# Performance work log

Hardware: AMD Instinct MI355X
Metric: run time of the kernel (lower is better)

Reference implementation:

```python
import jax, jax.numpy as jnp
import numpy as np

B, L, F = 16, 1080, 2
D = 128          # d_model
NC = 64          # num_cnn_channels
DIN = 256        # expand * d_model
N = 16           # d_state
K = 4            # d_conv
R = 8            # dt_rank = ceil(d_model/16)
OUT = 3
NB = 3           # num_mamba_blocks


def setup_inputs() -> dict:
    key = jax.random.key(0)
    ks = jax.random.split(key, 24)
    nrm = lambda k, shape, s=0.05: (jax.random.normal(k, shape) * s).astype(jnp.float32)
    bn = lambda c: jnp.stack([jnp.ones(c), jnp.zeros(c), jnp.zeros(c), jnp.ones(c)]).astype(jnp.float32)
    return {
        'x': jax.random.normal(ks[0], (B, L, F), dtype=jnp.float32),
        'emb_W': nrm(ks[1], (F, D), 0.5), 'emb_b': jnp.zeros(D, jnp.float32),
        'c3_W': nrm(ks[2], (NC, D, 3)), 'c3_b': jnp.zeros(NC, jnp.float32), 'bn3': bn(NC),
        'c5_W': nrm(ks[3], (NC, D, 5)), 'c5_b': jnp.zeros(NC, jnp.float32), 'bn5': bn(NC),
        'c7_W': nrm(ks[4], (NC, D, 7)), 'c7_b': jnp.zeros(NC, jnp.float32), 'bn7': bn(NC),
        'cf_W': nrm(ks[5], (D, 3 * NC, 1)), 'cf_b': jnp.zeros(D, jnp.float32), 'bnf': bn(D),
        'ln_g': jnp.ones((NB, D), jnp.float32), 'ln_b': jnp.zeros((NB, D), jnp.float32),
        'in_W': nrm(ks[6], (NB, 2 * DIN, D)),
        'mconv_W': nrm(ks[7], (NB, DIN, K), 0.2), 'mconv_b': jnp.zeros((NB, DIN), jnp.float32),
        'xproj_W': nrm(ks[8], (NB, R + 2 * N, DIN)),
        'dt_W': nrm(ks[9], (NB, DIN, R), 0.1), 'dt_b': jnp.full((NB, DIN), -1.0, jnp.float32),
        'A_log': jnp.tile(jnp.log(jnp.arange(1.0, N + 1.0, dtype=jnp.float32)), (NB, DIN, 1)),
        'Dp': jnp.ones((NB, DIN), jnp.float32),
        'out_W': nrm(ks[10], (NB, D, DIN)),
        'flin_W': nrm(ks[11], (D, 2 * D)), 'flin_b': jnp.zeros(D, jnp.float32),
        'fc_W': nrm(ks[12], (OUT, D)), 'fc_b': jnp.zeros(OUT, jnp.float32),
    }


def conv1d(x, W, b, pad):
    # x: (B,C,L), W: (O,C,K)
    y = jax.lax.conv_general_dilated(x, W, (1,), [(pad, pad)],
                                     dimension_numbers=('NCH', 'OIH', 'NCH'))
    return y + b[None, :, None]


def bn_relu(x, bn, eps=1e-5):
    g, b, m, v = bn  # each (C,)
    return jax.nn.relu((x - m[None, :, None]) * (g / jnp.sqrt(v + eps))[None, :, None] + b[None, :, None])


def layernorm(x, g, b, eps=1e-5):
    mu = x.mean(-1, keepdims=True)
    var = ((x - mu) ** 2).mean(-1, keepdims=True)
    return (x - mu) / jnp.sqrt(var + eps) * g + b


def pos_encoding(seq_len, d_model):
    pos = jnp.arange(seq_len, dtype=jnp.float32)[:, None]
    div = jnp.exp(jnp.arange(0, d_model, 2, dtype=jnp.float32) * (-np.log(10000.0) / d_model))
    pe = jnp.zeros((seq_len, d_model), jnp.float32)
    pe = pe.at[:, 0::2].set(jnp.sin(pos * div)).at[:, 1::2].set(jnp.cos(pos * div))
    return pe


def selective_scan(u, dt, A, Bm, Cm, Dp):
    # u,dt: (b,l,d); A: (d,n); Bm,Cm: (b,l,n); Dp: (d,)
    dA = jnp.exp(dt[..., None] * A)                    # (b,l,d,n)
    dBu = (dt * u)[..., None] * Bm[:, :, None, :]      # (b,l,d,n)

    def step(h, t):
        dA_t, dBu_t, C_t = t
        h = dA_t * h + dBu_t                           # (b,d,n)
        return h, jnp.einsum('bdn,bn->bd', h, C_t)

    h0 = jnp.zeros((u.shape[0], u.shape[2], A.shape[1]), u.dtype)
    _, ys = jax.lax.scan(step, h0, (jnp.swapaxes(dA, 0, 1), jnp.swapaxes(dBu, 0, 1), jnp.swapaxes(Cm, 0, 1)))
    return jnp.swapaxes(ys, 0, 1) + u * Dp


def mamba_block(x, in_W, conv_W, conv_b, xproj_W, dt_W, dt_b, A_log, Dp, out_W):
    xz = x @ in_W.T                                    # (b,l,2*din)
    xs, z = jnp.split(xz, 2, axis=-1)
    xc = jnp.swapaxes(xs, 1, 2)                        # (b,din,l)
    xc = jax.lax.conv_general_dilated(xc, conv_W[:, None, :], (1,), [(K - 1, 0)],
                                      dimension_numbers=('NCH', 'OIH', 'NCH'),
                                      feature_group_count=DIN)
    u = jax.nn.silu(jnp.swapaxes(xc + conv_b[None, :, None], 1, 2))  # (b,l,din)
    dbl = u @ xproj_W.T
    dt, Bm, Cm = dbl[..., :R], dbl[..., R:R + N], dbl[..., R + N:]
    dt = jax.nn.softplus(dt @ dt_W.T + dt_b)
    A = -jnp.exp(A_log)
    y = selective_scan(u, dt, A, Bm, Cm, Dp)
    return (y * jax.nn.silu(z)) @ out_W.T


def reference(x, emb_W, emb_b, c3_W, c3_b, bn3, c5_W, c5_b, bn5, c7_W, c7_b, bn7,
              cf_W, cf_b, bnf, ln_g, ln_b, in_W, mconv_W, mconv_b, xproj_W,
              dt_W, dt_b, A_log, Dp, out_W, flin_W, flin_b, fc_W, fc_b):
    xe = x @ emb_W + emb_b + pos_encoding(x.shape[1], emb_W.shape[1])  # (B,L,D)
    ci = jnp.swapaxes(xe, 1, 2)                                        # (B,D,L)
    o3 = bn_relu(conv1d(ci, c3_W, c3_b, 1), bn3)
    o5 = bn_relu(conv1d(ci, c5_W, c5_b, 2), bn5)
    o7 = bn_relu(conv1d(ci, c7_W, c7_b, 3), bn7)
    cc = jnp.concatenate([o3, o5, o7], axis=1)                         # (B,3*NC,L)
    cf = bn_relu(conv1d(cc, cf_W, cf_b, 0), bnf)
    cnn_feat = jnp.swapaxes(cf, 1, 2)                                  # (B,L,D)
    m = xe
    for i in range(NB):  # Sequential(LN, Mamba, Dropout) -- no residual, dropout=eval
        m = mamba_block(layernorm(m, ln_g[i], ln_b[i]), in_W[i], mconv_W[i], mconv_b[i],
                        xproj_W[i], dt_W[i], dt_b[i], A_log[i], Dp[i], out_W[i])
    fused = jax.nn.relu(jnp.concatenate([cnn_feat, m], axis=-1) @ flin_W.T + flin_b)
    pooled = fused.mean(axis=1)                                        # AdaptiveAvgPool1d(1)
    return pooled @ fc_W.T + fc_b
```

## Files before the change

kernel.cpp:

```cpp
#include <hip/hip_runtime.h>
#include <math.h>

#define LSEQ   1080
#define NBATCH 16
#define BLROWS (LSEQ*NBATCH)
#define CHN    27
#define LCH    40

typedef __bf16  bf16x8 __attribute__((ext_vector_type(8)));
typedef float   f32x4  __attribute__((ext_vector_type(4)));
typedef short   short8 __attribute__((ext_vector_type(8)));
typedef short   short4v __attribute__((ext_vector_type(4)));

__device__ __forceinline__ float silu_f(float x) { return x / (1.f + __expf(-x)); }

__device__ __forceinline__ unsigned short f2bf(float f) {
    unsigned int u = __float_as_uint(f);
    u += 0x7fffu + ((u >> 16) & 1u);
    return (unsigned short)(u >> 16);
}
__device__ __forceinline__ float bf2f(unsigned short h) {
    return __uint_as_float(((unsigned int)h) << 16);
}

__global__ __launch_bounds__(256) void embed_kernel(
    const float* __restrict__ x, const float* __restrict__ embW,
    const float* __restrict__ embb, float* __restrict__ xe)
{
    int idx = blockIdx.x * 256 + threadIdx.x;
    if (idx >= BLROWS * 128) return;
    int d = idx & 127;
    int r = idx >> 7;
    int t = r % LSEQ;
    float x0 = x[(size_t)r * 2], x1 = x[(size_t)r * 2 + 1];
    int i2 = d & 126;
    float div = expf((float)i2 * (-9.210340371976184f / 128.f));
    float arg = (float)t * div;
    float pe = (d & 1) ? cosf(arg) : sinf(arg);
    xe[idx] = fmaf(x0, embW[d], fmaf(x1, embW[128 + d], embb[d] + pe));
}

__global__ __launch_bounds__(256) void convw_kernel(
    const float* __restrict__ src, unsigned short* __restrict__ dh,
    unsigned short* __restrict__ dl, int NBk, int N, int Npad, int K)
{
    int idx = blockIdx.x * 256 + threadIdx.x;
    int total = NBk * Npad * K;
    if (idx >= total) return;
    int k = idx % K;
    int n = (idx / K) % Npad;
    int blk = idx / (K * Npad);
    float v = (n < N) ? src[((size_t)blk * N + n) * K + k] : 0.f;
    unsigned short h = f2bf(v);
    dh[idx] = h;
    dl[idx] = f2bf(v - bf2f(h));
}

__global__ __launch_bounds__(256) void convw_conv_kernel(
    const float* __restrict__ src, unsigned short* __restrict__ dh,
    unsigned short* __restrict__ dl, int T)
{
    int idx = blockIdx.x * 256 + threadIdx.x;
    int total = 64 * 128 * T;
    if (idx >= total) return;
    int kk = idx % (128 * T);
    int n = idx / (128 * T);
    int tap = kk / 128, d = kk % 128;
    float v = src[((size_t)n * 128 + d) * T + tap];
    unsigned short h = f2bf(v);
    dh[idx] = h;
    dl[idx] = f2bf(v - bf2f(h));
}

template<int BM, int BN>
__global__ __launch_bounds__(256) void gemm_mfma(
    const float* __restrict__ A, int lda,
    const unsigned short* __restrict__ Wh, const unsigned short* __restrict__ Wl,
    int Ntot, int Kd, int KT, int pad,
    const float* __restrict__ bias, const float* __restrict__ bn, int bnN, int epi,
    float* __restrict__ C, int ldc)
{
    constexpr int WM = BM / 2, WN = BN / 2;
    constexpr int MR = WM / 16, NR = WN / 16;
    constexpr int LA = (BM * 8) / 256;
    constexpr int LB = (BN * 4) / 256;

    __shared__ unsigned short Ah[BM][40], Al[BM][40];
    __shared__ unsigned short Bh[BN][40], Bl[BN][40];

    const int tid = threadIdx.x;
    const int b  = blockIdx.z;
    const int t0 = blockIdx.y * BM;
    const int n0 = blockIdx.x * BN;
    const float* Ab = A + (size_t)b * LSEQ * lda;
    const int wrow = Kd * KT;

    const int lane = tid & 63, wid = tid >> 6;
    const int wr = wid >> 1, wc = wid & 1;
    const int fr = lane & 15, fq = lane >> 4;

    f32x4 acc[MR][NR];
#pragma unroll
    for (int m = 0; m < MR; ++m)
#pragma unroll
        for (int n = 0; n < NR; ++n) acc[m][n] = (f32x4){0.f, 0.f, 0.f, 0.f};

    for (int tap = 0; tap < KT; ++tap) {
        const int shift = tap - pad;
        for (int ks = 0; ks < Kd; ks += 32) {
#pragma unroll
            for (int l = 0; l < LA; ++l) {
                int c = tid + l * 256;
                int row = c >> 3, kc = (c & 7) << 2;
                int ts = t0 + row + shift;
                float4 av = make_float4(0.f, 0.f, 0.f, 0.f);
                if (ts >= 0 && ts < LSEQ)
                    av = *(const float4*)(Ab + (size_t)ts * lda + ks + kc);
                alignas(8) unsigned short hs[4], ls[4];
                float fv[4] = {av.x, av.y, av.z, av.w};
#pragma unroll
                for (int j = 0; j < 4; ++j) {
                    unsigned short h = f2bf(fv[j]);
                    hs[j] = h;
                    ls[j] = f2bf(fv[j] - bf2f(h));
                }
                *(short4v*)&Ah[row][kc] = *(short4v*)hs;
                *(short4v*)&Al[row][kc] = *(short4v*)ls;
            }
            const int kglob = tap * Kd + ks;
#pragma unroll
            for (int l = 0; l < LB; ++l) {
                int c = tid + l * 256;
                int col = c >> 2, kc = (c & 3) << 3;
                size_t src = (size_t)(n0 + col) * wrow + kglob + kc;
                *(short8*)&Bh[col][kc] = *(const short8*)&Wh[src];
                *(short8*)&Bl[col][kc] = *(const short8*)&Wl[src];
            }
            __syncthreads();
            bf16x8 bhf[NR], blf[NR];
#pragma unroll
            for (int n = 0; n < NR; ++n) {
                int colr = wc * WN + n * 16 + fr;
                bhf[n] = __builtin_bit_cast(bf16x8, *(const short8*)&Bh[colr][fq * 8]);
                blf[n] = __builtin_bit_cast(bf16x8, *(const short8*)&Bl[colr][fq * 8]);
            }
#pragma unroll
            for (int m = 0; m < MR; ++m) {
                int rowr = wr * WM + m * 16 + fr;
                bf16x8 ahf = __builtin_bit_cast(bf16x8, *(const short8*)&Ah[rowr][fq * 8]);
                bf16x8 alf = __builtin_bit_cast(bf16x8, *(const short8*)&Al[rowr][fq * 8]);
#pragma unroll
                for (int n = 0; n < NR; ++n) {
                    acc[m][n] = __builtin_amdgcn_mfma_f32_16x16x32_bf16(ahf, bhf[n], acc[m][n], 0, 0, 0);
                    acc[m][n] = __builtin_amdgcn_mfma_f32_16x16x32_bf16(ahf, blf[n], acc[m][n], 0, 0, 0);
                    acc[m][n] = __builtin_amdgcn_mfma_f32_16x16x32_bf16(alf, bhf[n], acc[m][n], 0, 0, 0);
                }
            }
            __syncthreads();
        }
    }

    float* Cb = C + (size_t)b * LSEQ * ldc;
#pragma unroll
    for (int m = 0; m < MR; ++m) {
#pragma unroll
        for (int n = 0; n < NR; ++n) {
            int colg = n0 + wc * WN + n * 16 + fr;
            if (colg >= Ntot) continue;
#pragma unroll
            for (int r = 0; r < 4; ++r) {
                int t = t0 + wr * WM + m * 16 + fq * 4 + r;
                if (t >= LSEQ) continue;
                float v = acc[m][n][r];
                if (epi == 1) {
                    v += bias[colg];
                    float gg = bn[colg], bb = bn[bnN + colg];
                    float mm = bn[2 * bnN + colg], vv = bn[3 * bnN + colg];
                    v = (v - mm) * (gg / sqrtf(vv + 1e-5f)) + bb;
                    v = v > 0.f ? v : 0.f;
                } else if (epi == 2) {
                    v += bias[colg];
                    v = v > 0.f ? v : 0.f;
                }
                Cb[(size_t)t * ldc + colg] = v;
            }
        }
    }
}

__global__ __launch_bounds__(256) void ln_kernel(
    const float* __restrict__ in, const float* __restrict__ g,
    const float* __restrict__ b2, float* __restrict__ out)
{
    int lane = threadIdx.x & 63;
    int wid  = threadIdx.x >> 6;
    int row = blockIdx.x * 4 + wid;
    if (row >= BLROWS) return;
    const float* rp = in + (size_t)row * 128;
    float v0 = rp[lane], v1 = rp[lane + 64];
    float s = v0 + v1;
#pragma unroll
    for (int o2 = 32; o2 > 0; o2 >>= 1) s += __shfl_xor(s, o2, 64);
    float mu = s * (1.f / 128.f);
    float d0 = v0 - mu, d1 = v1 - mu;
    float q = d0 * d0 + d1 * d1;
#pragma unroll
    for (int o2 = 32; o2 > 0; o2 >>= 1) q += __shfl_xor(q, o2, 64);
    float rs = 1.f / sqrtf(q * (1.f / 128.f) + 1e-5f);
    float* op = out + (size_t)row * 128;
    op[lane]      = d0 * rs * g[lane]      + b2[lane];
    op[lane + 64] = d1 * rs * g[lane + 64] + b2[lane + 64];
}

__global__ __launch_bounds__(256) void mconv_kernel(
    const float* __restrict__ xz, const float* __restrict__ Wc,
    const float* __restrict__ bc, float* __restrict__ u)
{
    int idx = blockIdx.x * 256 + threadIdx.x;
    int c = idx & 255;
    int r = idx >> 8;
    if (r >= BLROWS) return;
    int t = r % LSEQ;
    const float* xs = xz + (size_t)r * 512 + c;
    float acc = bc[c];
    if (t >= 3) acc = fmaf(xs[-3 * 512], Wc[c * 4 + 0], acc);
    if (t >= 2) acc = fmaf(xs[-2 * 512], Wc[c * 4 + 1], acc);
    if (t >= 1) acc = fmaf(xs[-1 * 512], Wc[c * 4 + 2], acc);
    acc = fmaf(xs[0], Wc[c * 4 + 3], acc);
    u[(size_t)r * 256 + c] = silu_f(acc);
}

__global__ __launch_bounds__(256) void dtk_kernel(
    const float* __restrict__ dbl, const float* __restrict__ dtW,
    const float* __restrict__ dtb, float* __restrict__ dtout)
{
    int idx = blockIdx.x * 256 + threadIdx.x;
    int c = idx & 255;
    int r = idx >> 8;
    if (r >= BLROWS) return;
    const float* dr = dbl + (size_t)r * 40;
    float a = dtb[c];
#pragma unroll
    for (int j = 0; j < 8; ++j) a = fmaf(dr[j], dtW[c * 8 + j], a);
    float sp = (a > 20.f) ? a : log1pf(__expf(a));
    dtout[(size_t)r * 256 + c] = sp;
}

__global__ __launch_bounds__(256) void scan1_kernel(
    const float* __restrict__ dt, const float* __restrict__ u,
    const float* __restrict__ dbl, const float* __restrict__ Alog,
    float* __restrict__ P, float* __restrict__ S)
{
    int idx = blockIdx.x * 256 + threadIdx.x;
    int d = idx & 255;
    int rest = idx >> 8;
    int ch = rest % CHN;
    int b  = rest / CHN;
    float A2[16];
#pragma unroll
    for (int n = 0; n < 16; ++n) A2[n] = -__expf(Alog[d * 16 + n]);
    float p[16], s[16];
#pragma unroll
    for (int n = 0; n < 16; ++n) { p[n] = 1.f; s[n] = 0.f; }
    int r0 = b * LSEQ + ch * LCH;
    for (int q = 0; q < LCH; ++q) {
        size_t r = (size_t)(r0 + q);
        float dtv = dt[r * 256 + d];
        float uv  = u [r * 256 + d];
        float dtu = dtv * uv;
        const float* Br = dbl + r * 40 + 8;
#pragma unroll
        for (int n = 0; n < 16; ++n) {
            float a = __expf(dtv * A2[n]);
            p[n] *= a;
            s[n] = fmaf(a, s[n], dtu * Br[n]);
        }
    }
    size_t ob = ((size_t)(b * CHN + ch) * 256 + d) * 16;
#pragma unroll
    for (int n = 0; n < 16; ++n) { P[ob + n] = p[n]; S[ob + n] = s[n]; }
}

__global__ __launch_bounds__(256) void scan2_kernel(
    const float* __restrict__ P, const float* __restrict__ S, float* __restrict__ H0)
{
    int idx = blockIdx.x * 256 + threadIdx.x;
    int n = idx & 15;
    int d = (idx >> 4) & 255;
    int b = idx >> 12;
    float h = 0.f;
    for (int ch = 0; ch < CHN; ++ch) {
        size_t o = ((size_t)(b * CHN + ch) * 256 + d) * 16 + n;
        H0[o] = h;
        h = fmaf(P[o], h, S[o]);
    }
}

__global__ __launch_bounds__(256) void scan3_kernel(
    const float* __restrict__ dt, const float* __restrict__ u,
    const float* __restrict__ dbl, const float* __restrict__ Alog,
    const float* __restrict__ H0, const float* __restrict__ Dp,
    const float* __restrict__ xz, float* __restrict__ g)
{
    int idx = blockIdx.x * 256 + threadIdx.x;
    int d = idx & 255;
    int rest = idx >> 8;
    int ch = rest % CHN;
    int b  = rest / CHN;
    float A2[16];
#pragma unroll
    for (int n = 0; n < 16; ++n) A2[n] = -__expf(Alog[d * 16 + n]);
    float h[16];
    size_t ob = ((size_t)(b * CHN + ch) * 256 + d) * 16;
#pragma unroll
    for (int n = 0; n < 16; ++n) h[n] = H0[ob + n];
    float Dpd = Dp[d];
    int r0 = b * LSEQ + ch * LCH;
    for (int q = 0; q < LCH; ++q) {
        size_t r = (size_t)(r0 + q);
        float dtv = dt[r * 256 + d];
        float uv  = u [r * 256 + d];
        float dtu = dtv * uv;
        const float* Br = dbl + r * 40 + 8;
        const float* Cr = dbl + r * 40 + 24;
        float acc = 0.f;
#pragma unroll
        for (int n = 0; n < 16; ++n) {
            float a = __expf(dtv * A2[n]);
            h[n] = fmaf(a, h[n], dtu * Br[n]);
            acc = fmaf(h[n], Cr[n], acc);
        }
        float yv = fmaf(uv, Dpd, acc);
        float zv = xz[r * 512 + 256 + d];
        g[r * 256 + d] = yv * silu_f(zv);
    }
}

__global__ __launch_bounds__(128) void pool1_kernel(
    const float* __restrict__ fused, float* __restrict__ part)
{
    int d = threadIdx.x;
    int blk = blockIdx.x;
    int ch = blk % CHN;
    int b  = blk / CHN;
    int t0 = ch * LCH;
    float s = 0.f;
    for (int q = 0; q < LCH; ++q)
        s += fused[((size_t)(b * LSEQ + t0 + q)) * 128 + d];
    part[(size_t)(b * CHN + ch) * 128 + d] = s;
}

__global__ __launch_bounds__(128) void pool2_kernel(
    const float* __restrict__ part, const float* __restrict__ fcW,
    const float* __restrict__ fcb, float* __restrict__ out)
{
    __shared__ float pl[128];
    int d = threadIdx.x;
    int b = blockIdx.x;
    float s = 0.f;
    for (int ch = 0; ch < CHN; ++ch) s += part[(size_t)(b * CHN + ch) * 128 + d];
    pl[d] = s * (1.f / 1080.f);
    __syncthreads();
    if (d < 3) {
        float a = fcb[d];
        for (int dd = 0; dd < 128; ++dd) a = fmaf(pl[dd], fcW[d * 128 + dd], a);
        out[b * 3 + d] = a;
    }
}

extern "C" void kernel_launch(void* const* d_in, const int* in_sizes, int n_in,
                              void* d_out, int out_size, void* d_ws, size_t ws_size,
                              hipStream_t stream)
{
    const float* x    = (const float*)d_in[0];
    const float* embW = (const float*)d_in[1];
    const float* embb = (const float*)d_in[2];
    const float* c3W  = (const float*)d_in[3];
    const float* c3b  = (const float*)d_in[4];
    const float* bn3  = (const float*)d_in[5];
    const float* c5W  = (const float*)d_in[6];
    const float* c5b  = (const float*)d_in[7];
    const float* bn5  = (const float*)d_in[8];
    const float* c7W  = (const float*)d_in[9];
    const float* c7b  = (const float*)d_in[10];
    const float* bn7  = (const float*)d_in[11];
    const float* cfW  = (const float*)d_in[12];
    const float* cfb  = (const float*)d_in[13];
    const float* bnf  = (const float*)d_in[14];
    const float* lng  = (const float*)d_in[15];
    const float* lnb  = (const float*)d_in[16];
    const float* inW  = (const float*)d_in[17];
    const float* mcW  = (const float*)d_in[18];
    const float* mcb  = (const float*)d_in[19];
    const float* xpW  = (const float*)d_in[20];
    const float* dtW  = (const float*)d_in[21];
    const float* dtbp = (const float*)d_in[22];
    const float* Alog = (const float*)d_in[23];
    const float* Dp   = (const float*)d_in[24];
    const float* outW = (const float*)d_in[25];
    const float* flW  = (const float*)d_in[26];
    const float* flb  = (const float*)d_in[27];
    const float* fcW  = (const float*)d_in[28];
    const float* fcb  = (const float*)d_in[29];

    float* ws = (float*)d_ws;
    size_t off = 0;
    auto alloc = [&](size_t n) { float* p = ws + off; off += n; return p; };
    float* xe   = alloc((size_t)BLROWS * 128);
    float* lnx  = alloc((size_t)BLROWS * 128);
    float* xz   = alloc((size_t)BLROWS * 512);
    float* ub   = alloc((size_t)BLROWS * 256);
    float* dtt  = alloc((size_t)BLROWS * 256);
    float* dbl  = alloc((size_t)BLROWS * 40);
    float* gb   = alloc((size_t)BLROWS * 256);
    float* mbuf = alloc((size_t)BLROWS * 128);
    float* fin  = alloc((size_t)BLROWS * 256);
    float* Pb   = alloc((size_t)NBATCH * CHN * 256 * 16);
    float* Sb   = alloc((size_t)NBATCH * CHN * 256 * 16);
    float* h0b  = alloc((size_t)NBATCH * CHN * 256 * 16);
    float* cc    = gb;
    float* fused = lnx;

    off = (off + 3) & ~(size_t)3;
    unsigned short* us = (unsigned short*)(ws + off);
    size_t uo = 0;
    auto ualloc = [&](size_t n) { unsigned short* p = us + uo; uo += n; return p; };
    unsigned short* c3h = ualloc(64 * 384);  unsigned short* c3l = ualloc(64 * 384);
    unsigned short* c5h = ualloc(64 * 640);  unsigned short* c5l = ualloc(64 * 640);
    unsigned short* c7h = ualloc(64 * 896);  unsigned short* c7l = ualloc(64 * 896);
    unsigned short* cfh = ualloc(128 * 192); unsigned short* cfl = ualloc(128 * 192);
    unsigned short* inh = ualloc((size_t)1536 * 128); unsigned short* inl = ualloc((size_t)1536 * 128);
    unsigned short* xph = ualloc((size_t)3 * 64 * 256); unsigned short* xpl = ualloc((size_t)3 * 64 * 256);
    unsigned short* oth = ualloc((size_t)384 * 256); unsigned short* otl = ualloc((size_t)384 * 256);
    unsigned short* flh = ualloc((size_t)128 * 256); unsigned short* fll = ualloc((size_t)128 * 256);
    (void)ws_size; (void)in_sizes; (void)n_in; (void)out_size;

    convw_conv_kernel<<<(64 * 384 + 255) / 256, 256, 0, stream>>>(c3W, c3h, c3l, 3);
    convw_conv_kernel<<<(64 * 640 + 255) / 256, 256, 0, stream>>>(c5W, c5h, c5l, 5);
    convw_conv_kernel<<<(64 * 896 + 255) / 256, 256, 0, stream>>>(c7W, c7h, c7l, 7);
    convw_kernel<<<(128 * 192 + 255) / 256, 256, 0, stream>>>(cfW, cfh, cfl, 1, 128, 128, 192);
    convw_kernel<<<(1536 * 128 + 255) / 256, 256, 0, stream>>>(inW, inh, inl, 1, 1536, 1536, 128);
    convw_kernel<<<(3 * 64 * 256 + 255) / 256, 256, 0, stream>>>(xpW, xph, xpl, 3, 40, 64, 256);
    convw_kernel<<<(384 * 256 + 255) / 256, 256, 0, stream>>>(outW, oth, otl, 1, 384, 384, 256);
    convw_kernel<<<(128 * 256 + 255) / 256, 256, 0, stream>>>(flW, flh, fll, 1, 128, 128, 256);

    embed_kernel<<<(BLROWS * 128) / 256, 256, 0, stream>>>(x, embW, embb, xe);

    dim3 g64(1, 17, NBATCH);
    gemm_mfma<64, 64><<<g64, 256, 0, stream>>>(xe, 128, c3h, c3l, 64, 128, 3, 1,
                                               c3b, bn3, 64, 1, cc, 192);
    gemm_mfma<64, 64><<<g64, 256, 0, stream>>>(xe, 128, c5h, c5l, 64, 128, 5, 2,
                                               c5b, bn5, 64, 1, cc + 64, 192);
    gemm_mfma<64, 64><<<g64, 256, 0, stream>>>(xe, 128, c7h, c7l, 64, 128, 7, 3,
                                               c7b, bn7, 64, 1, cc + 128, 192);
    dim3 g128(1, 17, NBATCH);
    gemm_mfma<64, 128><<<g128, 256, 0, stream>>>(cc, 192, cfh, cfl, 128, 192, 1, 0,
                                                 cfb, bnf, 128, 1, fin, 256);

    for (int i = 0; i < 3; ++i) {
        const float* min_ = (i == 0) ? xe : ((i == 1) ? mbuf : xe);
        float* mout = (i == 0) ? mbuf : ((i == 1) ? xe : (fin + 128));
        int ldout = (i < 2) ? 128 : 256;

        ln_kernel<<<BLROWS / 4, 256, 0, stream>>>(min_, lng + i * 128, lnb + i * 128, lnx);

        dim3 gin(4, 17, NBATCH);
        gemm_mfma<64, 128><<<gin, 256, 0, stream>>>(lnx, 128, inh + (size_t)i * 512 * 128,
                                                    inl + (size_t)i * 512 * 128,
                                                    512, 128, 1, 0, nullptr, nullptr, 0, 0,
                                                    xz, 512);

        mconv_kernel<<<BLROWS, 256, 0, stream>>>(xz, mcW + i * 256 * 4, mcb + i * 256, ub);

        gemm_mfma<64, 64><<<g64, 256, 0, stream>>>(ub, 256, xph + (size_t)i * 64 * 256,
                                                   xpl + (size_t)i * 64 * 256,
                                                   40, 256, 1, 0, nullptr, nullptr, 0, 0,
                                                   dbl, 40);

        dtk_kernel<<<BLROWS, 256, 0, stream>>>(dbl, dtW + i * 256 * 8, dtbp + i * 256, dtt);

        scan1_kernel<<<(NBATCH * 256 * CHN) / 256, 256, 0, stream>>>(
            dtt, ub, dbl, Alog + i * 256 * 16, Pb, Sb);
        scan2_kernel<<<(NBATCH * 256 * 16) / 256, 256, 0, stream>>>(Pb, Sb, h0b);
        scan3_kernel<<<(NBATCH * 256 * CHN) / 256, 256, 0, stream>>>(
            dtt, ub, dbl, Alog + i * 256 * 16, h0b, Dp + i * 256, xz, gb);

        gemm_mfma<64, 128><<<g128, 256, 0, stream>>>(gb, 256, oth + (size_t)i * 128 * 256,
                                                     otl + (size_t)i * 128 * 256,
                                                     128, 256, 1, 0, nullptr, nullptr, 0, 0,
                                                     mout, ldout);
    }

    gemm_mfma<64, 128><<<g128, 256, 0, stream>>>(fin, 256, flh, fll, 128, 256, 1, 0,
                                                 flb, nullptr, 0, 2, fused, 128);

    pool1_kernel<<<NBATCH * CHN, 128, 0, stream>>>(fused, Pb);
    pool2_kernel<<<NBATCH, 128, 0, stream>>>(Pb, fcW, fcb, (float*)d_out);
}
```

Measured before the change: 795.8 us.

## Split scan state across 4 lanes, merge weight-convert and conv launches

The chunked selective-scan kernels now give each (batch, chunk, channel) four threads, each holding 4 of the 16 state elements. The partial C·h sums are combined with cross-lane shuffles, which raises parallelism from about 110K to 442K threads and cuts per-thread register use. Separately, the eight weight-conversion launches are merged into one kernel, and the three multi-tap conv GEMMs are merged into one launch that picks the branch from blockIdx.x. The scan change adds shuffle reductions and has each of the four threads reload dt and u, and only one lane in four writes the output.

```diff
diff --git a/kernel.cpp b/kernel.cpp
--- a/kernel.cpp
+++ b/kernel.cpp
@@ -40,45 +40,60 @@
     xe[idx] = fmaf(x0, embW[d], fmaf(x1, embW[128 + d], embb[d] + pe));
 }
 
-__global__ __launch_bounds__(256) void convw_kernel(
-    const float* __restrict__ src, unsigned short* __restrict__ dh,
-    unsigned short* __restrict__ dl, int NBk, int N, int Npad, int K)
-{
-    int idx = blockIdx.x * 256 + threadIdx.x;
-    int total = NBk * Npad * K;
-    if (idx >= total) return;
-    int k = idx % K;
-    int n = (idx / K) % Npad;
-    int blk = idx / (K * Npad);
-    float v = (n < N) ? src[((size_t)blk * N + n) * K + k] : 0.f;
+__global__ __launch_bounds__(256) void convw_all(
+    const float* __restrict__ c3W, const float* __restrict__ c5W,
+    const float* __restrict__ c7W, const float* __restrict__ cfW,
+    const float* __restrict__ inW, const float* __restrict__ xpW,
+    const float* __restrict__ otW, const float* __restrict__ flW,
+    unsigned short* __restrict__ c3h, unsigned short* __restrict__ c3l,
+    unsigned short* __restrict__ c5h, unsigned short* __restrict__ c5l,
+    unsigned short* __restrict__ c7h, unsigned short* __restrict__ c7l,
+    unsigned short* __restrict__ cfh, unsigned short* __restrict__ cfl,
+    unsigned short* __restrict__ inh, unsigned short* __restrict__ inl,
+    unsigned short* __restrict__ xph, unsigned short* __restrict__ xpl,
+    unsigned short* __restrict__ oth, unsigned short* __restrict__ otl,
+    unsigned short* __restrict__ flh, unsigned short* __restrict__ fll)
+{
+    int idx = blockIdx.x * 256 + threadIdx.x;
+    float v;
+    unsigned short *dh, *dl;
+    int off;
+    if (idx < 122880) {
+        const float* src; int T;
+        if (idx < 24576)      { src = c3W; T = 3; off = idx;          dh = c3h; dl = c3l; }
+        else if (idx < 65536) { src = c5W; T = 5; off = idx - 24576;  dh = c5h; dl = c5l; }
+        else                  { src = c7W; T = 7; off = idx - 65536;  dh = c7h; dl = c7l; }
+        int kk = off % (128 * T);
+        int n  = off / (128 * T);
+        int tap = kk / 128, d = kk % 128;
+        v = src[((size_t)n * 128 + d) * T + tap];
+    } else if (idx < 147456) {
+        off = idx - 122880; dh = cfh; dl = cfl; v = cfW[off];
+    } else if (idx < 344064) {
+        off = idx - 147456; dh = inh; dl = inl; v = inW[off];
+    } else if (idx < 393216) {
+        off = idx - 344064; dh = xph; dl = xpl;
+        int k = off % 256;
+        int n = (off / 256) % 64;
+        int blk = off / (256 * 64);
+        v = (n < 40) ? xpW[((size_t)blk * 40 + n) * 256 + k] : 0.f;
+    } else if (idx < 491520) {
+        off = idx - 393216; dh = oth; dl = otl; v = otW[off];
+    } else {
+        off = idx - 491520; dh = flh; dl = fll; v = flW[off];
+    }
     unsigned short h = f2bf(v);
-    dh[idx] = h;
-    dl[idx] = f2bf(v - bf2f(h));
-}
-
-__global__ __launch_bounds__(256) void convw_conv_kernel(
-    const float* __restrict__ src, unsigned short* __restrict__ dh,
-    unsigned short* __restrict__ dl, int T)
-{
-    int idx = blockIdx.x * 256 + threadIdx.x;
-    int total = 64 * 128 * T;
-    if (idx >= total) return;
-    int kk = idx % (128 * T);
-    int n = idx / (128 * T);
-    int tap = kk / 128, d = kk % 128;
-    float v = src[((size_t)n * 128 + d) * T + tap];
-    unsigned short h = f2bf(v);
-    dh[idx] = h;
-    dl[idx] = f2bf(v - bf2f(h));
+    dh[off] = h;
+    dl[off] = f2bf(v - bf2f(h));
 }
 
 template<int BM, int BN>
-__global__ __launch_bounds__(256) void gemm_mfma(
-    const float* __restrict__ A, int lda,
+__device__ __forceinline__ void gemm_body(
+    const float* __restrict__ Ab, int lda,
     const unsigned short* __restrict__ Wh, const unsigned short* __restrict__ Wl,
     int Ntot, int Kd, int KT, int pad,
     const float* __restrict__ bias, const float* __restrict__ bn, int bnN, int epi,
-    float* __restrict__ C, int ldc)
+    float* __restrict__ Cb, int ldc, int t0, int n0)
 {
     constexpr int WM = BM / 2, WN = BN / 2;
     constexpr int MR = WM / 16, NR = WN / 16;
@@ -89,12 +104,7 @@
     __shared__ unsigned short Bh[BN][40], Bl[BN][40];
 
     const int tid = threadIdx.x;
-    const int b  = blockIdx.z;
-    const int t0 = blockIdx.y * BM;
-    const int n0 = blockIdx.x * BN;
-    const float* Ab = A + (size_t)b * LSEQ * lda;
     const int wrow = Kd * KT;
-
     const int lane = tid & 63, wid = tid >> 6;
     const int wr = wid >> 1, wc = wid & 1;
     const int fr = lane & 15, fq = lane >> 4;
@@ -160,7 +170,6 @@
         }
     }
 
-    float* Cb = C + (size_t)b * LSEQ * ldc;
 #pragma unroll
     for (int m = 0; m < MR; ++m) {
 #pragma unroll
@@ -188,6 +197,42 @@
     }
 }
 
+template<int BM, int BN>
+__global__ __launch_bounds__(256) void gemm_mfma(
+    const float* __restrict__ A, int lda,
+    const unsigned short* __restrict__ Wh, const unsigned short* __restrict__ Wl,
+    int Ntot, int Kd, int KT, int pad,
+    const float* __restrict__ bias, const float* __restrict__ bn, int bnN, int epi,
+    float* __restrict__ C, int ldc)
+{
+    const int b = blockIdx.z;
+    gemm_body<BM, BN>(A + (size_t)b * LSEQ * lda, lda, Wh, Wl, Ntot, Kd, KT, pad,
+                      bias, bn, bnN, epi, C + (size_t)b * LSEQ * ldc, ldc,
+                      blockIdx.y * BM, blockIdx.x * BN);
+}
+
+__global__ __launch_bounds__(256) void convtri_mfma(
+    const float* __restrict__ A,
+    const unsigned short* __restrict__ c3h, const unsigned short* __restrict__ c3l,
+    const unsigned short* __restrict__ c5h, const unsigned short* __restrict__ c5l,
+    const unsigned short* __restrict__ c7h, const unsigned short* __restrict__ c7l,
+    const float* __restrict__ c3b, const float* __restrict__ c5b, const float* __restrict__ c7b,
+    const float* __restrict__ bn3, const float* __restrict__ bn5, const float* __restrict__ bn7,
+    float* __restrict__ C)
+{
+    const int br = blockIdx.x;
+    const int b  = blockIdx.z;
+    const int KT = 3 + 2 * br, pad = 1 + br;
+    const unsigned short* Wh = (br == 0) ? c3h : (br == 1) ? c5h : c7h;
+    const unsigned short* Wl = (br == 0) ? c3l : (br == 1) ? c5l : c7l;
+    const float* bias = (br == 0) ? c3b : (br == 1) ? c5b : c7b;
+    const float* bn   = (br == 0) ? bn3 : (br == 1) ? bn5 : bn7;
+    gemm_body<64, 64>(A + (size_t)b * LSEQ * 128, 128, Wh, Wl, 64, 128, KT, pad,
+                      bias, bn, 64, 1,
+                      C + (size_t)b * LSEQ * 192 + br * 64, 192,
+                      blockIdx.y * 64, 0);
+}
+
 __global__ __launch_bounds__(256) void ln_kernel(
     const float* __restrict__ in, const float* __restrict__ g,
     const float* __restrict__ b2, float* __restrict__ out)
@@ -252,33 +297,34 @@
     float* __restrict__ P, float* __restrict__ S)
 {
     int idx = blockIdx.x * 256 + threadIdx.x;
-    int d = idx & 255;
-    int rest = idx >> 8;
+    int ng = idx & 3;
+    int d  = (idx >> 2) & 255;
+    int rest = idx >> 10;
     int ch = rest % CHN;
     int b  = rest / CHN;
-    float A2[16];
-#pragma unroll
-    for (int n = 0; n < 16; ++n) A2[n] = -__expf(Alog[d * 16 + n]);
-    float p[16], s[16];
-#pragma unroll
-    for (int n = 0; n < 16; ++n) { p[n] = 1.f; s[n] = 0.f; }
+    int n0 = ng * 4;
+    float A2[4];
+#pragma unroll
+    for (int j = 0; j < 4; ++j) A2[j] = -__expf(Alog[d * 16 + n0 + j]);
+    float p[4] = {1.f, 1.f, 1.f, 1.f}, s[4] = {0.f, 0.f, 0.f, 0.f};
     int r0 = b * LSEQ + ch * LCH;
     for (int q = 0; q < LCH; ++q) {
         size_t r = (size_t)(r0 + q);
         float dtv = dt[r * 256 + d];
         float uv  = u [r * 256 + d];
         float dtu = dtv * uv;
-        const float* Br = dbl + r * 40 + 8;
-#pragma unroll
-        for (int n = 0; n < 16; ++n) {
-            float a = __expf(dtv * A2[n]);
-            p[n] *= a;
-            s[n] = fmaf(a, s[n], dtu * Br[n]);
+        float4 Br = *(const float4*)(dbl + r * 40 + 8 + n0);
+        float bv[4] = {Br.x, Br.y, Br.z, Br.w};
+#pragma unroll
+        for (int j = 0; j < 4; ++j) {
+            float a = __expf(dtv * A2[j]);
+            p[j] *= a;
+            s[j] = fmaf(a, s[j], dtu * bv[j]);
         }
     }
-    size_t ob = ((size_t)(b * CHN + ch) * 256 + d) * 16;
-#pragma unroll
-    for (int n = 0; n < 16; ++n) { P[ob + n] = p[n]; S[ob + n] = s[n]; }
+    size_t ob = ((size_t)(b * CHN + ch) * 256 + d) * 16 + n0;
+    *(float4*)&P[ob] = make_float4(p[0], p[1], p[2], p[3]);
+    *(float4*)&S[ob] = make_float4(s[0], s[1], s[2], s[3]);
 }
 
 __global__ __launch_bounds__(256) void scan2_kernel(
@@ -303,17 +349,18 @@
     const float* __restrict__ xz, float* __restrict__ g)
 {
     int idx = blockIdx.x * 256 + threadIdx.x;
-    int d = idx & 255;
-    int rest = idx >> 8;
+    int ng = idx & 3;
+    int d  = (idx >> 2) & 255;
+    int rest = idx >> 10;
     int ch = rest % CHN;
     int b  = rest / CHN;
-    float A2[16];
-#pragma unroll
-    for (int n = 0; n < 16; ++n) A2[n] = -__expf(Alog[d * 16 + n]);
-    float h[16];
-    size_t ob = ((size_t)(b * CHN + ch) * 256 + d) * 16;
-#pragma unroll
-    for (int n = 0; n < 16; ++n) h[n] = H0[ob + n];
+    int n0 = ng * 4;
+    float A2[4];
+#pragma unroll
+    for (int j = 0; j < 4; ++j) A2[j] = -__expf(Alog[d * 16 + n0 + j]);
+    size_t ob = ((size_t)(b * CHN + ch) * 256 + d) * 16 + n0;
+    float4 h4 = *(const float4*)&H0[ob];
+    float h[4] = {h4.x, h4.y, h4.z, h4.w};
     float Dpd = Dp[d];
     int r0 = b * LSEQ + ch * LCH;
     for (int q = 0; q < LCH; ++q) {
@@ -321,18 +368,24 @@
         float dtv = dt[r * 256 + d];
         float uv  = u [r * 256 + d];
         float dtu = dtv * uv;
-        const float* Br = dbl + r * 40 + 8;
-        const float* Cr = dbl + r * 40 + 24;
-        float acc = 0.f;
-#pragma unroll
-        for (int n = 0; n < 16; ++n) {
-            float a = __expf(dtv * A2[n]);
-            h[n] = fmaf(a, h[n], dtu * Br[n]);
-            acc = fmaf(h[n], Cr[n], acc);
+        float4 Br = *(const float4*)(dbl + r * 40 + 8 + n0);
+        float4 Cr = *(const float4*)(dbl + r * 40 + 24 + n0);
+        float bv[4] = {Br.x, Br.y, Br.z, Br.w};
+        float cv[4] = {Cr.x, Cr.y, Cr.z, Cr.w};
+        float pacc = 0.f;
+#pragma unroll
+        for (int j = 0; j < 4; ++j) {
+            float a = __expf(dtv * A2[j]);
+            h[j] = fmaf(a, h[j], dtu * bv[j]);
+            pacc = fmaf(h[j], cv[j], pacc);
         }
-        float yv = fmaf(uv, Dpd, acc);
-        float zv = xz[r * 512 + 256 + d];
-        g[r * 256 + d] = yv * silu_f(zv);
+        float acc = pacc + __shfl_xor(pacc, 1);
+        acc += __shfl_xor(acc, 2);
+        if (ng == 0) {
+            float yv = fmaf(uv, Dpd, acc);
+            float zv = xz[r * 512 + 256 + d];
+            g[r * 256 + d] = yv * silu_f(zv);
+        }
     }
 }
 
@@ -435,24 +488,16 @@
     unsigned short* flh = ualloc((size_t)128 * 256); unsigned short* fll = ualloc((size_t)128 * 256);
     (void)ws_size; (void)in_sizes; (void)n_in; (void)out_size;
 
-    convw_conv_kernel<<<(64 * 384 + 255) / 256, 256, 0, stream>>>(c3W, c3h, c3l, 3);
-    convw_conv_kernel<<<(64 * 640 + 255) / 256, 256, 0, stream>>>(c5W, c5h, c5l, 5);
-    convw_conv_kernel<<<(64 * 896 + 255) / 256, 256, 0, stream>>>(c7W, c7h, c7l, 7);
-    convw_kernel<<<(128 * 192 + 255) / 256, 256, 0, stream>>>(cfW, cfh, cfl, 1, 128, 128, 192);
-    convw_kernel<<<(1536 * 128 + 255) / 256, 256, 0, stream>>>(inW, inh, inl, 1, 1536, 1536, 128);
-    convw_kernel<<<(3 * 64 * 256 + 255) / 256, 256, 0, stream>>>(xpW, xph, xpl, 3, 40, 64, 256);
-    convw_kernel<<<(384 * 256 + 255) / 256, 256, 0, stream>>>(outW, oth, otl, 1, 384, 384, 256);
-    convw_kernel<<<(128 * 256 + 255) / 256, 256, 0, stream>>>(flW, flh, fll, 1, 128, 128, 256);
+    convw_all<<<2048, 256, 0, stream>>>(c3W, c5W, c7W, cfW, inW, xpW, outW, flW,
+                                        c3h, c3l, c5h, c5l, c7h, c7l, cfh, cfl,
+                                        inh, inl, xph, xpl, oth, otl, flh, fll);
 
     embed_kernel<<<(BLROWS * 128) / 256, 256, 0, stream>>>(x, embW, embb, xe);
 
+    dim3 gtri(3, 17, NBATCH);
+    convtri_mfma<<<gtri, 256, 0, stream>>>(xe, c3h, c3l, c5h, c5l, c7h, c7l,
+                                           c3b, c5b, c7b, bn3, bn5, bn7, cc);
     dim3 g64(1, 17, NBATCH);
-    gemm_mfma<64, 64><<<g64, 256, 0, stream>>>(xe, 128, c3h, c3l, 64, 128, 3, 1,
-                                               c3b, bn3, 64, 1, cc, 192);
-    gemm_mfma<64, 64><<<g64, 256, 0, stream>>>(xe, 128, c5h, c5l, 64, 128, 5, 2,
-                                               c5b, bn5, 64, 1, cc + 64, 192);
-    gemm_mfma<64, 64><<<g64, 256, 0, stream>>>(xe, 128, c7h, c7l, 64, 128, 7, 3,
-                                               c7b, bn7, 64, 1, cc + 128, 192);
     dim3 g128(1, 17, NBATCH);
     gemm_mfma<64, 128><<<g128, 256, 0, stream>>>(cc, 192, cfh, cfl, 128, 192, 1, 0,
                                                  cfb, bnf, 128, 1, fin, 256);
@@ -479,10 +524,10 @@
 
         dtk_kernel<<<BLROWS, 256, 0, stream>>>(dbl, dtW + i * 256 * 8, dtbp + i * 256, dtt);
 
-        scan1_kernel<<<(NBATCH * 256 * CHN) / 256, 256, 0, stream>>>(
+        scan1_kernel<<<(NBATCH * CHN * 1024) / 256, 256, 0, stream>>>(
             dtt, ub, dbl, Alog + i * 256 * 16, Pb, Sb);
         scan2_kernel<<<(NBATCH * 256 * 16) / 256, 256, 0, stream>>>(Pb, Sb, h0b);
-        scan3_kernel<<<(NBATCH * 256 * CHN) / 256, 256, 0, stream>>>(
+        scan3_kernel<<<(NBATCH * CHN * 1024) / 256, 256, 0, stream>>>(
             dtt, ub, dbl, Alog + i * 256 * 16, h0b, Dp + i * 256, xz, gb);
 
         gemm_mfma<64, 128><<<g128, 256, 0, stream>>>(gb, 256, oth + (size_t)i * 128 * 256,
```

After: 682.0 us. 1.17x faster.
